# Performance work log

Hardware: AMD Instinct MI355X
Metric: run time of the kernel (lower is better)

Reference implementation:

```python
import jax, jax.numpy as jnp
import numpy as np

B_SZ = 4; SEQ = 2048; SPLIT = 1024
D_MODEL = 512; N_LAYERS = 2; EXPAND = 2
D_INNER = EXPAND * D_MODEL          # 1024
HEADDIM = 64; NHEADS = D_INNER // HEADDIM   # 16
DSTATE = 64; CONV = 4; CHUNK = 256
D_INPROJ = 2 * D_INNER + 2 * DSTATE + NHEADS   # z, xBC, dt
CONVDIM = D_INNER + 2 * DSTATE
NHID = 1024; NOUT = 10; CA_HEADS = 4; CA_HD = D_MODEL // CA_HEADS


def _ln(x, w, b, eps=1e-5):
    m = jnp.mean(x, -1, keepdims=True)
    v = jnp.mean(jnp.square(x - m), -1, keepdims=True)
    return (x - m) * jax.lax.rsqrt(v + eps) * w + b


def _segsum(x):
    # x: (..., T) -> (..., T, T) lower-triangular cumulative segment sums
    T = x.shape[-1]
    xc = jnp.cumsum(x, -1)
    ss = xc[..., :, None] - xc[..., None, :]
    mask = jnp.tril(jnp.ones((T, T), bool))
    return jnp.where(mask, ss, -jnp.inf)


def _ssd(x, A, B, C):
    # chunked SSD (Mamba2). x:(b,l,h,p) dt-prescaled; A:(b,l,h)=dt*A; B,C:(b,l,n)
    b, l, h, p = x.shape
    n = B.shape[-1]
    c = l // CHUNK
    x = x.reshape(b, c, CHUNK, h, p)
    A = jnp.transpose(A.reshape(b, c, CHUNK, h), (0, 1, 3, 2))   # (b,c,h,L)
    B = B.reshape(b, c, CHUNK, n)
    C = C.reshape(b, c, CHUNK, n)
    A_cum = jnp.cumsum(A, -1)
    Lmat = jnp.exp(_segsum(A))                                    # (b,c,h,L,L)
    Y_diag = jnp.einsum('bcln,bcsn,bchls,bcshp->bclhp', C, B, Lmat, x)
    decay_states = jnp.exp(A_cum[..., -1:] - A_cum)               # (b,c,h,L)
    states = jnp.einsum('bcln,bchl,bclhp->bchpn', B, decay_states, x)
    chunk_decay = jnp.exp(A_cum[..., -1])                         # (b,c,h)
    def step(hprev, inp):
        dec, s = inp
        return hprev * dec[..., None, None] + s, hprev
    init = jnp.zeros((b, h, p, n), x.dtype)
    _, prev = jax.lax.scan(step, init,
                           (jnp.moveaxis(chunk_decay, 1, 0), jnp.moveaxis(states, 1, 0)))
    prev = jnp.moveaxis(prev, 0, 1)                               # (b,c,h,p,n) state at chunk start
    Y_off = jnp.einsum('bcln,bchpn,bchl->bclhp', C, prev, jnp.exp(A_cum))
    return (Y_diag + Y_off).reshape(b, l, h, p)


def _mamba2_dir(u, Win, cw, cb, dtb, Alog, Dp, gw, Wout):
    b, l, _ = u.shape
    zxbcdt = u @ Win
    z, xBC, dt_raw = jnp.split(zxbcdt, [D_INNER, D_INNER + CONVDIM], -1)
    # causal depthwise conv, kernel CONV
    xp = jnp.pad(xBC, ((0, 0), (CONV - 1, 0), (0, 0)))
    xc = cb + sum(xp[:, k:k + l, :] * cw[:, k] for k in range(CONV))
    xc = jax.nn.silu(xc)
    x, Bm, Cm = jnp.split(xc, [D_INNER, D_INNER + DSTATE], -1)
    dt = jax.nn.softplus(dt_raw + dtb)                            # (b,l,h)
    A = -jnp.exp(Alog)                                            # (h,)
    xh = x.reshape(b, l, NHEADS, HEADDIM)
    y = _ssd(xh * dt[..., None], dt * A, Bm, Cm) + Dp[None, None, :, None] * xh
    y = y.reshape(b, l, D_INNER) * jax.nn.silu(z)                 # gated
    y = y * jax.lax.rsqrt(jnp.mean(jnp.square(y), -1, keepdims=True) + 1e-5) * gw
    return y @ Wout


def _cross_attn(q_in, c_in, nqw, nqb, nkvw, nkvb, qw, qb, kw, kb, vw, vb, ow, ob):
    res = q_in
    q = _ln(q_in, nqw, nqb)
    c = _ln(c_in, nkvw, nkvb)
    Bq, Nq, D = q.shape
    Nc = c.shape[1]
    Q = (q @ qw + qb).reshape(Bq, Nq, CA_HEADS, CA_HD)
    K = (c @ kw + kb).reshape(Bq, Nc, CA_HEADS, CA_HD)
    V = (c @ vw + vb).reshape(Bq, Nc, CA_HEADS, CA_HD)
    attn = jax.nn.softmax(jnp.einsum('bqhd,bkhd->bhqk', Q, K) / np.float32(np.sqrt(CA_HD)), -1)
    out = jnp.einsum('bhqk,bkhd->bqhd', attn, V).reshape(Bq, Nq, D)
    return res + out @ ow + ob


def _forward(x_enc, split_pos, in_proj_w, conv_w, conv_b, dt_bias, A_log, D_param,
             gnorm_w, out_proj_w, norm_w, norm_b, normf_w, normf_b,
             ca_nq_w, ca_nq_b, ca_nkv_w, ca_nkv_b, ca_qw, ca_qb, ca_kw, ca_kb,
             ca_vw, ca_vb, ca_ow, ca_ob, qp_w, qp_b, cp_w, cp_b,
             dec1_w, dec1_b, dec2_w, dec2_b):
    h = x_enc
    res = None
    for i in range(N_LAYERS):
        res = h if res is None else h + res
        hn = _ln(res, norm_w[i], norm_b[i])
        fwd = _mamba2_dir(hn, in_proj_w[i, 0], conv_w[i, 0], conv_b[i, 0], dt_bias[i, 0],
                          A_log[i, 0], D_param[i, 0], gnorm_w[i, 0], out_proj_w[i, 0])
        bwd = _mamba2_dir(jnp.flip(hn, 1), in_proj_w[i, 1], conv_w[i, 1], conv_b[i, 1],
                          dt_bias[i, 1], A_log[i, 1], D_param[i, 1], gnorm_w[i, 1], out_proj_w[i, 1])
        h = fwd + jnp.flip(bwd, 1)
    res = h + res
    h = _ln(res, normf_w, normf_b)
    context = h[:, :split_pos]
    query = h[:, split_pos:]
    q = query @ qp_w + qp_b
    c = context @ cp_w + cp_b
    out = _cross_attn(q, c, ca_nq_w, ca_nq_b, ca_nkv_w, ca_nkv_b,
                      ca_qw, ca_qb, ca_kw, ca_kb, ca_vw, ca_vb, ca_ow, ca_ob)
    out = jax.nn.gelu(out @ dec1_w + dec1_b, approximate=False) @ dec2_w + dec2_b
    return out


def setup_inputs() -> dict:
    key = jax.random.key(0)
    ks = iter(jax.random.split(key, 64))
    def nrm(shape, scale=0.02):
        return jax.random.normal(next(ks), shape, jnp.float32) * scale
    L2 = (N_LAYERS, 2)
    inp = {}
    inp['x_enc'] = jax.random.normal(next(ks), (B_SZ, SEQ, D_MODEL), jnp.float32)
    inp['split_pos'] = SPLIT
    inp['in_proj_w'] = nrm(L2 + (D_MODEL, D_INPROJ))
    inp['conv_w'] = nrm(L2 + (CONVDIM, CONV), 0.1)
    inp['conv_b'] = jnp.zeros(L2 + (CONVDIM,), jnp.float32)
    inp['dt_bias'] = nrm(L2 + (NHEADS,), 0.5)
    inp['A_log'] = jnp.log(jnp.broadcast_to(jnp.arange(1, NHEADS + 1, dtype=jnp.float32), L2 + (NHEADS,)))
    inp['D_param'] = jnp.ones(L2 + (NHEADS,), jnp.float32)
    inp['gnorm_w'] = jnp.ones(L2 + (D_INNER,), jnp.float32)
    inp['out_proj_w'] = nrm(L2 + (D_INNER, D_MODEL))
    inp['norm_w'] = jnp.ones((N_LAYERS, D_MODEL), jnp.float32)
    inp['norm_b'] = jnp.zeros((N_LAYERS, D_MODEL), jnp.float32)
    inp['normf_w'] = jnp.ones((D_MODEL,), jnp.float32)
    inp['normf_b'] = jnp.zeros((D_MODEL,), jnp.float32)
    inp['ca_nq_w'] = jnp.ones((D_MODEL,), jnp.float32); inp['ca_nq_b'] = jnp.zeros((D_MODEL,), jnp.float32)
    inp['ca_nkv_w'] = jnp.ones((D_MODEL,), jnp.float32); inp['ca_nkv_b'] = jnp.zeros((D_MODEL,), jnp.float32)
    for nm in ['ca_qw', 'ca_kw', 'ca_vw', 'ca_ow']:
        inp[nm] = nrm((D_MODEL, D_MODEL))
    for nm in ['ca_qb', 'ca_kb', 'ca_vb', 'ca_ob']:
        inp[nm] = jnp.zeros((D_MODEL,), jnp.float32)
    inp['qp_w'] = nrm((D_MODEL, D_MODEL)); inp['qp_b'] = jnp.zeros((D_MODEL,), jnp.float32)
    inp['cp_w'] = nrm((D_MODEL, D_MODEL)); inp['cp_b'] = jnp.zeros((D_MODEL,), jnp.float32)
    inp['dec1_w'] = nrm((D_MODEL, NHID)); inp['dec1_b'] = jnp.zeros((NHID,), jnp.float32)
    inp['dec2_w'] = nrm((NHID, NOUT)); inp['dec2_b'] = jnp.zeros((NOUT,), jnp.float32)
    return inp


def reference(x_enc, split_pos, in_proj_w, conv_w, conv_b, dt_bias, A_log, D_param,
              gnorm_w, out_proj_w, norm_w, norm_b, normf_w, normf_b,
              ca_nq_w, ca_nq_b, ca_nkv_w, ca_nkv_b, ca_qw, ca_qb, ca_kw, ca_kb,
              ca_vw, ca_vb, ca_ow, ca_ob, qp_w, qp_b, cp_w, cp_b,
              dec1_w, dec1_b, dec2_w, dec2_b):
    return _forward(x_enc, split_pos, in_proj_w, conv_w, conv_b, dt_bias, A_log, D_param,
                    gnorm_w, out_proj_w, norm_w, norm_b, normf_w, normf_b,
                    ca_nq_w, ca_nq_b, ca_nkv_w, ca_nkv_b, ca_qw, ca_qb, ca_kw, ca_kb,
                    ca_vw, ca_vb, ca_ow, ca_ob, qp_w, qp_b, cp_w, cp_b,
                    dec1_w, dec1_b, dec2_w, dec2_b)
```

## Files before the change

kernel.cpp:

```cpp
#include <hip/hip_runtime.h>
#include <hip/hip_bf16.h>

#define BS 4
#define SEQL 2048
#define DM 512
#define DIN 1024
#define NH 16
#define HD 64
#define DST 64
#define NC 8
#define CKS 256
#define DIP 2192
#define CVD 1152
#define NROWS (BS*SEQL)
#define NTOK (BS*SEQL*DM)

typedef unsigned short u16;
typedef __bf16 bf16x8 __attribute__((ext_vector_type(8)));
typedef float f32x4 __attribute__((ext_vector_type(4)));

__device__ __forceinline__ u16 cvt_bf16(float f){
  unsigned int x = __float_as_uint(f);
  unsigned int r = x + 0x7fffu + ((x>>16)&1u);
  return (u16)(r>>16);
}
__device__ __forceinline__ float bf2f(u16 u){
  return __uint_as_float(((unsigned int)u)<<16);
}

__global__ void k_add_flip(float* __restrict__ dst, const float* __restrict__ src, int flip){
  int i = blockIdx.x*256 + threadIdx.x;
  if(i >= NTOK) return;
  int d = i & (DM-1);
  int l = (i >> 9) & (SEQL-1);
  int b = i >> 20;
  int sl = flip ? (SEQL-1-l) : l;
  dst[i] += src[(b*SEQL + sl)*DM + d];
}

__global__ void k_flip(float* __restrict__ dst, const float* __restrict__ src){
  int i = blockIdx.x*256 + threadIdx.x;
  if(i >= NTOK) return;
  int d = i & (DM-1);
  int l = (i >> 9) & (SEQL-1);
  int b = i >> 20;
  dst[i] = src[(b*SEQL + (SEQL-1-l))*DM + d];
}

__global__ void k_cvt(const float* __restrict__ src, u16* __restrict__ dst, int n4){
  int i = blockIdx.x*256 + threadIdx.x;
  if(i >= n4) return;
  float4 f = reinterpret_cast<const float4*>(src)[i];
  ushort4 o; o.x=cvt_bf16(f.x); o.y=cvt_bf16(f.y); o.z=cvt_bf16(f.z); o.w=cvt_bf16(f.w);
  reinterpret_cast<ushort4*>(dst)[i] = o;
}

__global__ void k_ln(const float* __restrict__ X, const float* __restrict__ w,
                     const float* __restrict__ bb, float* __restrict__ O){
  int row = blockIdx.x, tid = threadIdx.x;
  const float* x = X + (size_t)row*DM;
  float* o = O + (size_t)row*DM;
  float s=0.f, s2=0.f;
  for(int j=tid;j<DM;j+=256){ float v=x[j]; s+=v; s2+=v*v; }
  __shared__ float r1[256], r2[256];
  r1[tid]=s; r2[tid]=s2; __syncthreads();
  for(int off=128;off>0;off>>=1){
    if(tid<off){ r1[tid]+=r1[tid+off]; r2[tid]+=r2[tid+off]; }
    __syncthreads();
  }
  float m = r1[0]*(1.f/DM);
  float var = r2[0]*(1.f/DM) - m*m;
  float inv = rsqrtf(var + 1e-5f);
  for(int j=tid;j<DM;j+=256) o[j] = (x[j]-m)*inv*w[j] + bb[j];
}

__global__ void k_rmsb(const float* __restrict__ Y, const float* __restrict__ gw,
                       u16* __restrict__ Obf){
  int row = blockIdx.x, tid = threadIdx.x;
  const float* y = Y + (size_t)row*DIN;
  float ss=0.f;
  for(int j=tid;j<DIN;j+=256){ float v=y[j]; ss+=v*v; }
  __shared__ float red[256];
  red[tid]=ss; __syncthreads();
  for(int off=128;off>0;off>>=1){
    if(tid<off) red[tid]+=red[tid+off];
    __syncthreads();
  }
  float inv = rsqrtf(red[0]*(1.f/DIN) + 1e-5f);
  for(int j=tid;j<DIN;j+=256) Obf[(size_t)row*DIN + j] = cvt_bf16(y[j]*inv*gw[j]);
}

__global__ void k_dec2(const float* __restrict__ D1, const float* __restrict__ w,
                       const float* __restrict__ bb, float* __restrict__ out){
  int row = blockIdx.x, tid = threadIdx.x;
  int lane = tid & 63, wave = tid >> 6;
  const float* x = D1 + (size_t)row*1024;
  float acc[10];
  #pragma unroll
  for(int o=0;o<10;o++) acc[o]=0.f;
  for(int j=tid;j<1024;j+=256){
    float v = x[j];
    const float* wr = w + (size_t)j*10;
    #pragma unroll
    for(int o=0;o<10;o++) acc[o] += v*wr[o];
  }
  __shared__ float red[4][10];
  #pragma unroll
  for(int o=0;o<10;o++){
    float v = acc[o];
    #pragma unroll
    for(int s=32;s>0;s>>=1) v += __shfl_down(v, s, 64);
    if(lane==0) red[wave][o] = v;
  }
  __syncthreads();
  if(tid < 10)
    out[(size_t)row*10 + tid] = red[0][tid]+red[1][tid]+red[2][tid]+red[3][tid] + bb[tid];
}

__global__ void k_wt2(const float* __restrict__ src, u16* __restrict__ dst,
                      int K, int N, int lds){
  __shared__ float t[32][33];
  int n0 = blockIdx.x*32, k0 = blockIdx.y*32;
  int tx = threadIdx.x, ty = threadIdx.y;
  #pragma unroll
  for(int i=0;i<32;i+=8){
    int k = k0+ty+i, n = n0+tx;
    t[ty+i][tx] = (n<N) ? src[(size_t)k*lds+n] : 0.f;
  }
  __syncthreads();
  #pragma unroll
  for(int i=0;i<32;i+=8){
    int n = n0+ty+i, k = k0+tx;
    if(n<N) dst[(size_t)n*K+k] = cvt_bf16(t[tx][ty+i]);
  }
}

__global__ void k_vtb(const float* __restrict__ VV, u16* __restrict__ VT){
  __shared__ float t[32][33];
  int z = blockIdx.z, b = z>>2, h = z&3;
  const float* src = VV + (size_t)b*524288 + h*128;
  u16* dst = VT + (size_t)z*131072;
  int n0 = blockIdx.x*32, k0 = blockIdx.y*32;
  int tx = threadIdx.x, ty = threadIdx.y;
  #pragma unroll
  for(int i=0;i<32;i+=8){
    int k = k0+ty+i, n = n0+tx;
    t[ty+i][tx] = src[(size_t)k*512+n];
  }
  __syncthreads();
  #pragma unroll
  for(int i=0;i<32;i+=8){
    int n = n0+ty+i, k = k0+tx;
    dst[(size_t)n*1024+k] = cvt_bf16(t[tx][ty+i]);
  }
}

__global__ void k_xdtt(const float* __restrict__ XC, const float* __restrict__ DT,
                       u16* __restrict__ XdT){
  __shared__ float t[32][33];
  int z = blockIdx.z;
  int h = z & 15, bc = z >> 4;
  int b = bc >> 3, c = bc & 7;
  int p0 = blockIdx.x*32, s0 = blockIdx.y*32;
  int tx = threadIdx.x, ty = threadIdx.y;
  int gbase = b*SEQL + c*CKS;
  #pragma unroll
  for(int i=0;i<32;i+=8){
    int s = s0+ty+i, p = p0+tx;
    int g = gbase + s;
    t[ty+i][tx] = XC[(size_t)g*CVD + h*HD + p] * DT[(size_t)g*NH + h];
  }
  __syncthreads();
  u16* dst = XdT + (size_t)z*16384;
  #pragma unroll
  for(int i=0;i<32;i+=8){
    int p = p0+ty+i, s = s0+tx;
    dst[(size_t)p*256 + s] = cvt_bf16(t[tx][ty+i]);
  }
}

__global__ void k_btc(const u16* __restrict__ Bbf, u16* __restrict__ BTc){
  __shared__ u16 t[32][33];
  int bc = blockIdx.z;
  const u16* src = Bbf + (size_t)bc*16384;
  u16* dst = BTc + (size_t)bc*16384;
  int n0 = blockIdx.x*32, l0 = blockIdx.y*32;
  int tx = threadIdx.x, ty = threadIdx.y;
  #pragma unroll
  for(int i=0;i<32;i+=8){
    int l = l0+ty+i, n = n0+tx;
    t[ty+i][tx] = src[(size_t)l*64+n];
  }
  __syncthreads();
  #pragma unroll
  for(int i=0;i<32;i+=8){
    int n = n0+ty+i, l = l0+tx;
    dst[(size_t)n*256+l] = t[tx][ty+i];
  }
}

__global__ __launch_bounds__(256) void k_mg(
    const u16* __restrict__ A, const u16* __restrict__ BT,
    float* __restrict__ C, int M, int N, int K, int lda, int ldb, int ldc)
{
  __shared__ u16 As[128*32];
  __shared__ u16 Bs[128*32];
  const int tid = threadIdx.x;
  const int row0 = blockIdx.y*128, col0 = blockIdx.x*128;
  const int lane = tid & 63, wave = tid >> 6;
  const int wm = wave >> 1, wn = wave & 1;
  const int lr = lane & 15, ksg = (lane >> 4);
  const int srow = lane >> 2;
  const int slot = lane & 3;
  f32x4 acc[4][4];
  #pragma unroll
  for(int i=0;i<4;i++)
    #pragma unroll
    for(int j=0;j<4;j++) acc[i][j] = (f32x4){0.f,0.f,0.f,0.f};
  for(int k0=0;k0<K;k0+=32){
    #pragma unroll
    for(int i=0;i<2;i++){
      int seg = wave*2 + i;
      int row = seg*16 + srow;
      int kk  = slot ^ ((row>>1)&3);
      const u16* ga = A + (size_t)(row0+row)*lda + k0 + kk*8;
      __builtin_amdgcn_global_load_lds(
        (const __attribute__((address_space(1))) void*)ga,
        (__attribute__((address_space(3))) void*)&As[seg*512], 16, 0, 0);
      int bcol = col0 + row; if(bcol > N-1) bcol = N-1;
      const u16* gb = BT + (size_t)bcol*ldb + k0 + kk*8;
      __builtin_amdgcn_global_load_lds(
        (const __attribute__((address_space(1))) void*)gb,
        (__attribute__((address_space(3))) void*)&Bs[seg*512], 16, 0, 0);
    }
    __syncthreads();
    bf16x8 afr[4], bfr[4];
    #pragma unroll
    for(int i=0;i<4;i++){
      int ar = wm*64+i*16+lr;
      afr[i] = *reinterpret_cast<const bf16x8*>(&As[ar*32 + (ksg^((ar>>1)&3))*8]);
    }
    #pragma unroll
    for(int j=0;j<4;j++){
      int br = wn*64+j*16+lr;
      bfr[j] = *reinterpret_cast<const bf16x8*>(&Bs[br*32 + (ksg^((br>>1)&3))*8]);
    }
    #pragma unroll
    for(int i=0;i<4;i++)
      #pragma unroll
      for(int j=0;j<4;j++)
        acc[i][j] = __builtin_amdgcn_mfma_f32_16x16x32_bf16(afr[i], bfr[j], acc[i][j], 0, 0, 0);
    __syncthreads();
  }
  const int hi = lane >> 4, lo = lane & 15;
  #pragma unroll
  for(int i=0;i<4;i++)
    #pragma unroll
    for(int j=0;j<4;j++)
      #pragma unroll
      for(int r=0;r<4;r++){
        int row = row0 + wm*64 + i*16 + 4*hi + r;
        int col = col0 + wn*64 + j*16 + lo;
        if(col < N) C[(size_t)row*ldc + col] = acc[i][j][r];
      }
}

__global__ __launch_bounds__(256) void k_mgo(
    const u16* __restrict__ A, const u16* __restrict__ BT,
    float* __restrict__ H, int flip)
{
  const int N = 512, K = 1024;
  __shared__ u16 As[128*32];
  __shared__ u16 Bs[128*32];
  const int tid = threadIdx.x;
  const int row0 = blockIdx.y*128, col0 = blockIdx.x*128;
  const int lane = tid & 63, wave = tid >> 6;
  const int wm = wave >> 1, wn = wave & 1;
  const int lr = lane & 15, ksg = (lane >> 4);
  const int srow = lane >> 2;
  const int slot = lane & 3;
  f32x4 acc[4][4];
  #pragma unroll
  for(int i=0;i<4;i++)
    #pragma unroll
    for(int j=0;j<4;j++) acc[i][j] = (f32x4){0.f,0.f,0.f,0.f};
  for(int k0=0;k0<K;k0+=32){
    #pragma unroll
    for(int i=0;i<2;i++){
      int seg = wave*2 + i;
      int row = seg*16 + srow;
      int kk  = slot ^ ((row>>1)&3);
      const u16* ga = A + (size_t)(row0+row)*K + k0 + kk*8;
      __builtin_amdgcn_global_load_lds(
        (const __attribute__((address_space(1))) void*)ga,
        (__attribute__((address_space(3))) void*)&As[seg*512], 16, 0, 0);
      int bcol = col0 + row; if(bcol > N-1) bcol = N-1;
      const u16* gb = BT + (size_t)bcol*K + k0 + kk*8;
      __builtin_amdgcn_global_load_lds(
        (const __attribute__((address_space(1))) void*)gb,
        (__attribute__((address_space(3))) void*)&Bs[seg*512], 16, 0, 0);
    }
    __syncthreads();
    bf16x8 afr[4], bfr[4];
    #pragma unroll
    for(int i=0;i<4;i++){
      int ar = wm*64+i*16+lr;
      afr[i] = *reinterpret_cast<const bf16x8*>(&As[ar*32 + (ksg^((ar>>1)&3))*8]);
    }
    #pragma unroll
    for(int j=0;j<4;j++){
      int br = wn*64+j*16+lr;
      bfr[j] = *reinterpret_cast<const bf16x8*>(&Bs[br*32 + (ksg^((br>>1)&3))*8]);
    }
    #pragma unroll
    for(int i=0;i<4;i++)
      #pragma unroll
      for(int j=0;j<4;j++)
        acc[i][j] = __builtin_amdgcn_mfma_f32_16x16x32_bf16(afr[i], bfr[j], acc[i][j], 0, 0, 0);
    __syncthreads();
  }
  const int hi = lane >> 4, lo = lane & 15;
  #pragma unroll
  for(int i=0;i<4;i++)
    #pragma unroll
    for(int j=0;j<4;j++)
      #pragma unroll
      for(int r=0;r<4;r++){
        int row = row0 + wm*64 + i*16 + 4*hi + r;
        int col = col0 + wn*64 + j*16 + lo;
        if(col < N){
          int b = row >> 11, l = row & (SEQL-1);
          int sl = flip ? (SEQL-1-l) : l;
          size_t ci = (size_t)(b*SEQL + sl)*DM + col;
          H[ci] += acc[i][j][r];
        }
      }
}

__global__ __launch_bounds__(256) void k_mgb(
    const u16* __restrict__ A0, const u16* __restrict__ BT0,
    float* __restrict__ C0, int M, int N, int K, int lda, int ldb, int ldc,
    long sAz, long sBz, long sCo, long sCi, int shC)
{
  const int z = blockIdx.z;
  const u16* A  = A0  + (size_t)z*sAz;
  const u16* BT = BT0 + (size_t)z*sBz;
  float* C = C0 + (size_t)(z>>shC)*sCo + (size_t)(z & ((1<<shC)-1))*sCi;
  __shared__ uint4 As4[128*5];
  __shared__ uint4 Bs4[128*5];
  const int tid = threadIdx.x;
  const int row0 = blockIdx.y*128, col0 = blockIdx.x*128;
  const int lane = tid & 63, wave = tid >> 6;
  const int wm = wave >> 1, wn = wave & 1;
  const int lr = lane & 15, ksg = (lane >> 4);
  f32x4 acc[4][4];
  #pragma unroll
  for(int i=0;i<4;i++)
    #pragma unroll
    for(int j=0;j<4;j++) acc[i][j] = (f32x4){0.f,0.f,0.f,0.f};
  for(int k0=0;k0<K;k0+=32){
    #pragma unroll
    for(int i=0;i<2;i++){
      int t2 = tid + i*256;
      int rr = t2 >> 2, sg = (t2 & 3);
      uint4 av = *reinterpret_cast<const uint4*>(A + (size_t)(row0+rr)*lda + k0 + sg*8);
      uint4 bv = {0u,0u,0u,0u};
      if(col0+rr < N) bv = *reinterpret_cast<const uint4*>(BT + (size_t)(col0+rr)*ldb + k0 + sg*8);
      As4[rr*5 + sg] = av;
      Bs4[rr*5 + sg] = bv;
    }
    __syncthreads();
    bf16x8 afr[4], bfr[4];
    #pragma unroll
    for(int i=0;i<4;i++) afr[i] = *reinterpret_cast<const bf16x8*>(&As4[(wm*64+i*16+lr)*5 + ksg]);
    #pragma unroll
    for(int j=0;j<4;j++) bfr[j] = *reinterpret_cast<const bf16x8*>(&Bs4[(wn*64+j*16+lr)*5 + ksg]);
    #pragma unroll
    for(int i=0;i<4;i++)
      #pragma unroll
      for(int j=0;j<4;j++)
        acc[i][j] = __builtin_amdgcn_mfma_f32_16x16x32_bf16(afr[i], bfr[j], acc[i][j], 0, 0, 0);
    __syncthreads();
  }
  const int hi = lane >> 4, lo = lane & 15;
  #pragma unroll
  for(int i=0;i<4;i++)
    #pragma unroll
    for(int j=0;j<4;j++)
      #pragma unroll
      for(int r=0;r<4;r++){
        int row = row0 + wm*64 + i*16 + 4*hi + r;
        int col = col0 + wn*64 + j*16 + lo;
        if(col < N) C[(size_t)row*ldc + col] = acc[i][j][r];
      }
}

__global__ __launch_bounds__(256) void k_mgg(
    const float* __restrict__ Sf, const float* __restrict__ ACUM,
    const u16* __restrict__ XdT, float* __restrict__ Y)
{
  const int z = blockIdx.z;
  const int h = z & 15, bc = z >> 4;
  const int b = bc >> 3, c = bc & 7;
  const float* Az = Sf + (size_t)bc*65536;
  const float* Acp = ACUM + (size_t)z*256;
  const u16* BT = XdT + (size_t)z*16384;
  float* Cp = Y + (size_t)b*2097152 + (size_t)c*262144 + h*64;
  __shared__ uint4 As4[128*5];
  __shared__ uint4 Bs4[128*5];
  __shared__ float AcS[256];
  const int tid = threadIdx.x;
  AcS[tid] = Acp[tid];
  __syncthreads();
  const int row0 = blockIdx.y*128;
  const int lane = tid & 63, wave = tid >> 6;
  const int wm = wave >> 1, wn = wave & 1;
  const int lr = lane & 15, ksg = (lane >> 4);
  f32x4 acc[4][4];
  #pragma unroll
  for(int i=0;i<4;i++)
    #pragma unroll
    for(int j=0;j<4;j++) acc[i][j] = (f32x4){0.f,0.f,0.f,0.f};
  for(int k0=0;k0<256;k0+=32){
    #pragma unroll
    for(int i=0;i<2;i++){
      int t2 = tid + i*256;
      int rr = t2 >> 2, sg = (t2 & 3);
      int l = row0 + rr;
      int sbase = k0 + sg*8;
      float4 v0 = *reinterpret_cast<const float4*>(Az + (size_t)l*256 + sbase);
      float4 v1 = *reinterpret_cast<const float4*>(Az + (size_t)l*256 + sbase + 4);
      float acl = AcS[l];
      float vv[8] = {v0.x,v0.y,v0.z,v0.w,v1.x,v1.y,v1.z,v1.w};
      u16 gbuf[8];
      #pragma unroll
      for(int e=0;e<8;e++){
        int s = sbase + e;
        float g = 0.f;
        if(s <= l) g = __expf(acl - AcS[s]) * vv[e];
        gbuf[e] = cvt_bf16(g);
      }
      As4[rr*5 + sg] = *reinterpret_cast<uint4*>(gbuf);
      uint4 bv = {0u,0u,0u,0u};
      if(rr < 64) bv = *reinterpret_cast<const uint4*>(BT + (size_t)rr*256 + sbase);
      Bs4[rr*5 + sg] = bv;
    }
    __syncthreads();
    bf16x8 afr[4], bfr[4];
    #pragma unroll
    for(int i=0;i<4;i++) afr[i] = *reinterpret_cast<const bf16x8*>(&As4[(wm*64+i*16+lr)*5 + ksg]);
    #pragma unroll
    for(int j=0;j<4;j++) bfr[j] = *reinterpret_cast<const bf16x8*>(&Bs4[(wn*64+j*16+lr)*5 + ksg]);
    #pragma unroll
    for(int i=0;i<4;i++)
      #pragma unroll
      for(int j=0;j<4;j++)
        acc[i][j] = __builtin_amdgcn_mfma_f32_16x16x32_bf16(afr[i], bfr[j], acc[i][j], 0, 0, 0);
    __syncthreads();
  }
  const int hi = lane >> 4, lo = lane & 15;
  #pragma unroll
  for(int i=0;i<4;i++)
    #pragma unroll
    for(int j=0;j<4;j++)
      #pragma unroll
      for(int r=0;r<4;r++){
        int row = row0 + wm*64 + i*16 + 4*hi + r;
        int col = wn*64 + j*16 + lo;
        if(col < 64) Cp[(size_t)row*1024 + col] = acc[i][j][r];
      }
}

__global__ __launch_bounds__(256) void k_mgs(
    const u16* __restrict__ XdT, const u16* __restrict__ BTc,
    const float* __restrict__ ACUM, float* __restrict__ ST)
{
  const int z = blockIdx.z;
  const int bc = z >> 4;
  const u16* Ap = XdT + (size_t)z*16384;
  const u16* BT = BTc + (size_t)bc*16384;
  float* Cp = ST + (size_t)z*4096;
  __shared__ uint4 As4[128*5];
  __shared__ uint4 Bs4[128*5];
  __shared__ float decS[256];
  const int tid = threadIdx.x;
  {
    const float* Acp = ACUM + (size_t)z*256;
    decS[tid] = __expf(Acp[255] - Acp[tid]);
  }
  __syncthreads();
  const int lane = tid & 63, wave = tid >> 6;
  const int wm = wave >> 1, wn = wave & 1;
  const int lr = lane & 15, ksg = (lane >> 4);
  f32x4 acc[4][4];
  #pragma unroll
  for(int i=0;i<4;i++)
    #pragma unroll
    for(int j=0;j<4;j++) acc[i][j] = (f32x4){0.f,0.f,0.f,0.f};
  for(int k0=0;k0<256;k0+=32){
    #pragma unroll
    for(int i=0;i<2;i++){
      int t2 = tid + i*256;
      int rr = t2 >> 2, sg = (t2 & 3);
      int sbase = k0 + sg*8;
      uint4 av = {0u,0u,0u,0u};
      if(rr < 64){
        uint4 raw = *reinterpret_cast<const uint4*>(Ap + (size_t)rr*256 + sbase);
        const u16* rp = reinterpret_cast<const u16*>(&raw);
        u16 buf[8];
        #pragma unroll
        for(int e=0;e<8;e++) buf[e] = cvt_bf16(bf2f(rp[e]) * decS[sbase+e]);
        av = *reinterpret_cast<uint4*>(buf);
      }
      As4[rr*5 + sg] = av;
      uint4 bv = {0u,0u,0u,0u};
      if(rr < 64) bv = *reinterpret_cast<const uint4*>(BT + (size_t)rr*256 + sbase);
      Bs4[rr*5 + sg] = bv;
    }
    __syncthreads();
    bf16x8 afr[4], bfr[4];
    #pragma unroll
    for(int i=0;i<4;i++) afr[i] = *reinterpret_cast<const bf16x8*>(&As4[(wm*64+i*16+lr)*5 + ksg]);
    #pragma unroll
    for(int j=0;j<4;j++) bfr[j] = *reinterpret_cast<const bf16x8*>(&Bs4[(wn*64+j*16+lr)*5 + ksg]);
    #pragma unroll
    for(int i=0;i<4;i++)
      #pragma unroll
      for(int j=0;j<4;j++)
        acc[i][j] = __builtin_amdgcn_mfma_f32_16x16x32_bf16(afr[i], bfr[j], acc[i][j], 0, 0, 0);
    __syncthreads();
  }
  const int hi = lane >> 4, lo = lane & 15;
  #pragma unroll
  for(int i=0;i<4;i++)
    #pragma unroll
    for(int j=0;j<4;j++)
      #pragma unroll
      for(int r=0;r<4;r++){
        int row = wm*64 + i*16 + 4*hi + r;
        int col = wn*64 + j*16 + lo;
        if(row < 64 && col < 64) Cp[(size_t)row*64 + col] = acc[i][j][r];
      }
}

__global__ __launch_bounds__(256) void k_mgab(
    const u16* __restrict__ A0, const u16* __restrict__ BT0,
    float* __restrict__ C0, u16* __restrict__ Cb0,
    int M, int N, int K, int lda, int ldb, int ldc,
    long sAo, long sAi, long sBo, long sBi, long sCo, long sCi, float scale)
{
  const int z = blockIdx.z;
  const u16* A  = A0  + (size_t)(z>>2)*sAo + (size_t)(z&3)*sAi;
  const u16* BT = BT0 + (size_t)(z>>2)*sBo + (size_t)(z&3)*sBi;
  const size_t offC = (size_t)(z>>2)*sCo + (size_t)(z&3)*sCi;
  __shared__ uint4 As4[128*5];
  __shared__ uint4 Bs4[128*5];
  const int tid = threadIdx.x;
  const int row0 = blockIdx.y*128, col0 = blockIdx.x*128;
  const int lane = tid & 63, wave = tid >> 6;
  const int wm = wave >> 1, wn = wave & 1;
  const int lr = lane & 15, ksg = (lane >> 4);
  f32x4 acc[4][4];
  #pragma unroll
  for(int i=0;i<4;i++)
    #pragma unroll
    for(int j=0;j<4;j++) acc[i][j] = (f32x4){0.f,0.f,0.f,0.f};
  for(int k0=0;k0<K;k0+=32){
    #pragma unroll
    for(int i=0;i<2;i++){
      int t2 = tid + i*256;
      int rr = t2 >> 2, sg = (t2 & 3);
      uint4 av = *reinterpret_cast<const uint4*>(A + (size_t)(row0+rr)*lda + k0 + sg*8);
      uint4 bv = {0u,0u,0u,0u};
      if(col0+rr < N) bv = *reinterpret_cast<const uint4*>(BT + (size_t)(col0+rr)*ldb + k0 + sg*8);
      As4[rr*5 + sg] = av;
      Bs4[rr*5 + sg] = bv;
    }
    __syncthreads();
    bf16x8 afr[4], bfr[4];
    #pragma unroll
    for(int i=0;i<4;i++) afr[i] = *reinterpret_cast<const bf16x8*>(&As4[(wm*64+i*16+lr)*5 + ksg]);
    #pragma unroll
    for(int j=0;j<4;j++) bfr[j] = *reinterpret_cast<const bf16x8*>(&Bs4[(wn*64+j*16+lr)*5 + ksg]);
    #pragma unroll
    for(int i=0;i<4;i++)
      #pragma unroll
      for(int j=0;j<4;j++)
        acc[i][j] = __builtin_amdgcn_mfma_f32_16x16x32_bf16(afr[i], bfr[j], acc[i][j], 0, 0, 0);
    __syncthreads();
  }
  const int hi = lane >> 4, lo = lane & 15;
  #pragma unroll
  for(int i=0;i<4;i++)
    #pragma unroll
    for(int j=0;j<4;j++)
      #pragma unroll
      for(int r=0;r<4;r++){
        int row = row0 + wm*64 + i*16 + 4*hi + r;
        int col = col0 + wn*64 + j*16 + lo;
        if(col < N){
          float v = acc[i][j][r] * scale;
          size_t ci = offC + (size_t)row*ldc + col;
          if(C0) C0[ci] = v;
          else   Cb0[ci] = cvt_bf16(v);
        }
      }
}

__global__ __launch_bounds__(256) void k_mgy(
    const u16* __restrict__ Cb0, const u16* __restrict__ PV0,
    const float* __restrict__ ACUM, const float* __restrict__ XCp,
    const float* __restrict__ ZBp, const float* __restrict__ Dp,
    float* __restrict__ Y)
{
  const int z = blockIdx.z;
  const int b = z>>3, c = z&7;
  const u16* A  = Cb0 + (size_t)z*16384;
  const u16* BT = PV0 + (size_t)z*65536;
  const int N = 1024;
  __shared__ uint4 As4[128*5];
  __shared__ uint4 Bs4[128*5];
  const int tid = threadIdx.x;
  const int row0 = blockIdx.y*128, col0 = blockIdx.x*128;
  const int lane = tid & 63, wave = tid >> 6;
  const int wm = wave >> 1, wn = wave & 1;
  const int lr = lane & 15, ksg = (lane >> 4);
  f32x4 acc[4][4];
  #pragma unroll
  for(int i=0;i<4;i++)
    #pragma unroll
    for(int j=0;j<4;j++) acc[i][j] = (f32x4){0.f,0.f,0.f,0.f};
  for(int k0=0;k0<64;k0+=32){
    #pragma unroll
    for(int i=0;i<2;i++){
      int t2 = tid + i*256;
      int rr = t2 >> 2, sg = (t2 & 3);
      uint4 av = *reinterpret_cast<const uint4*>(A + (size_t)(row0+rr)*64 + k0 + sg*8);
      uint4 bv = {0u,0u,0u,0u};
      if(col0+rr < N) bv = *reinterpret_cast<const uint4*>(BT + (size_t)(col0+rr)*64 + k0 + sg*8);
      As4[rr*5 + sg] = av;
      Bs4[rr*5 + sg] = bv;
    }
    __syncthreads();
    bf16x8 afr[4], bfr[4];
    #pragma unroll
    for(int i=0;i<4;i++) afr[i] = *reinterpret_cast<const bf16x8*>(&As4[(wm*64+i*16+lr)*5 + ksg]);
    #pragma unroll
    for(int j=0;j<4;j++) bfr[j] = *reinterpret_cast<const bf16x8*>(&Bs4[(wn*64+j*16+lr)*5 + ksg]);
    #pragma unroll
    for(int i=0;i<4;i++)
      #pragma unroll
      for(int j=0;j<4;j++)
        acc[i][j] = __builtin_amdgcn_mfma_f32_16x16x32_bf16(afr[i], bfr[j], acc[i][j], 0, 0, 0);
    __syncthreads();
  }
  const int hi = lane >> 4, lo = lane & 15;
  #pragma unroll
  for(int i=0;i<4;i++)
    #pragma unroll
    for(int j=0;j<4;j++)
      #pragma unroll
      for(int r=0;r<4;r++){
        int row = row0 + wm*64 + i*16 + 4*hi + r;
        int col = col0 + wn*64 + j*16 + lo;
        int h = col >> 6;
        int g = b*SEQL + c*CKS + row;
        float ac = ACUM[((size_t)z*NH + h)*CKS + row];
        float xh = XCp[(size_t)g*CVD + col];
        float zg = ZBp[(size_t)g*DIP + col];
        size_t ci = (size_t)g*DIN + col;
        float v = Y[ci] + expf(ac)*acc[i][j][r] + Dp[h]*xh;
        float sig = 1.f/(1.f+expf(-zg));
        Y[ci] = v * (zg*sig);
      }
}

__global__ __launch_bounds__(256) void k_mge(
    const u16* __restrict__ A, const u16* __restrict__ BT,
    const float* __restrict__ bias, const float* __restrict__ res,
    float* __restrict__ C, u16* __restrict__ Cbf,
    int M, int N, int K, int lda, int ldb, int ldc, float scale, int act)
{
  __shared__ uint4 As4[128*5];
  __shared__ uint4 Bs4[128*5];
  const int tid = threadIdx.x;
  const int row0 = blockIdx.y*128, col0 = blockIdx.x*128;
  const int lane = tid & 63, wave = tid >> 6;
  const int wm = wave >> 1, wn = wave & 1;
  const int lr = lane & 15, ksg = (lane >> 4);
  f32x4 acc[4][4];
  #pragma unroll
  for(int i=0;i<4;i++)
    #pragma unroll
    for(int j=0;j<4;j++) acc[i][j] = (f32x4){0.f,0.f,0.f,0.f};
  for(int k0=0;k0<K;k0+=32){
    #pragma unroll
    for(int i=0;i<2;i++){
      int t2 = tid + i*256;
      int rr = t2 >> 2, sg = (t2 & 3);
      uint4 av = *reinterpret_cast<const uint4*>(A + (size_t)(row0+rr)*lda + k0 + sg*8);
      uint4 bv = {0u,0u,0u,0u};
      if(col0+rr < N) bv = *reinterpret_cast<const uint4*>(BT + (size_t)(col0+rr)*ldb + k0 + sg*8);
      As4[rr*5 + sg] = av;
      Bs4[rr*5 + sg] = bv;
    }
    __syncthreads();
    bf16x8 afr[4], bfr[4];
    #pragma unroll
    for(int i=0;i<4;i++) afr[i] = *reinterpret_cast<const bf16x8*>(&As4[(wm*64+i*16+lr)*5 + ksg]);
    #pragma unroll
    for(int j=0;j<4;j++) bfr[j] = *reinterpret_cast<const bf16x8*>(&Bs4[(wn*64+j*16+lr)*5 + ksg]);
    #pragma unroll
    for(int i=0;i<4;i++)
      #pragma unroll
      for(int j=0;j<4;j++)
        acc[i][j] = __builtin_amdgcn_mfma_f32_16x16x32_bf16(afr[i], bfr[j], acc[i][j], 0, 0, 0);
    __syncthreads();
  }
  const int hi = lane >> 4, lo = lane & 15;
  #pragma unroll
  for(int i=0;i<4;i++)
    #pragma unroll
    for(int j=0;j<4;j++)
      #pragma unroll
      for(int r=0;r<4;r++){
        int row = row0 + wm*64 + i*16 + 4*hi + r;
        int col = col0 + wn*64 + j*16 + lo;
        if(col < N){
          float v = acc[i][j][r];
          if(bias) v += bias[col];
          v *= scale;
          if(act==1) v = 0.5f*v*(1.f+erff(v*0.70710678118654752f));
          size_t ci = (size_t)row*ldc + col;
          if(res) v += res[ci];
          if(C) C[ci] = v;
          else  Cbf[ci] = cvt_bf16(v);
        }
      }
}

__global__ void k_sm(u16* __restrict__ S){
  size_t row = blockIdx.x;
  u16* p = S + row*1024;
  int tid = threadIdx.x;
  ushort4 u = reinterpret_cast<ushort4*>(p)[tid];
  float v0=bf2f(u.x), v1=bf2f(u.y), v2=bf2f(u.z), v3=bf2f(u.w);
  float m = fmaxf(fmaxf(v0,v1),fmaxf(v2,v3));
  __shared__ float red[256];
  red[tid]=m; __syncthreads();
  for(int o=128;o>0;o>>=1){ if(tid<o) red[tid]=fmaxf(red[tid],red[tid+o]); __syncthreads(); }
  m = red[0]; __syncthreads();
  v0=__expf(v0-m); v1=__expf(v1-m); v2=__expf(v2-m); v3=__expf(v3-m);
  float s = v0+v1+v2+v3;
  red[tid]=s; __syncthreads();
  for(int o=128;o>0;o>>=1){ if(tid<o) red[tid]+=red[tid+o]; __syncthreads(); }
  float inv = 1.f/red[0];
  ushort4 o4; o4.x=cvt_bf16(v0*inv); o4.y=cvt_bf16(v1*inv); o4.z=cvt_bf16(v2*inv); o4.w=cvt_bf16(v3*inv);
  reinterpret_cast<ushort4*>(p)[tid] = o4;
}

__global__ void k_conv4(const float* __restrict__ ZB, const float* __restrict__ cw,
                        const float* __restrict__ cb, float* __restrict__ XC){
  int i = blockIdx.x*256 + threadIdx.x;
  if(i >= BS*512*CVD) return;
  int cch = i % CVD;
  int lq = (i / CVD) & 511;
  int b = i / (CVD*512);
  int l0 = lq*4;
  float w[7];
  #pragma unroll
  for(int t=0;t<7;t++){
    int sl = l0 - 3 + t;
    w[t] = (sl >= 0) ? ZB[(size_t)(b*SEQL+sl)*DIP + DIN + cch] : 0.f;
  }
  float c0 = cw[cch*4+0], c1 = cw[cch*4+1], c2 = cw[cch*4+2], c3 = cw[cch*4+3];
  float bb2 = cb[cch];
  #pragma unroll
  for(int j=0;j<4;j++){
    float v = bb2 + w[j]*c0 + w[j+1]*c1 + w[j+2]*c2 + w[j+3]*c3;
    float sig = 1.f/(1.f+expf(-v));
    XC[(size_t)(b*SEQL + l0 + j)*CVD + cch] = v*sig;
  }
}

__global__ void k_dt(const float* __restrict__ ZB, const float* __restrict__ dtb,
                     const float* __restrict__ Alog, float* __restrict__ DT,
                     float* __restrict__ DA){
  int i = blockIdx.x*256 + threadIdx.x;
  if(i >= BS*SEQL*NH) return;
  int h = i & (NH-1);
  int row = i >> 4;
  float raw = ZB[(size_t)row*DIP + (DIN+CVD) + h] + dtb[h];
  float dt = fmaxf(raw,0.f) + log1pf(expf(-fabsf(raw)));
  DT[i] = dt;
  DA[i] = dt * (-expf(Alog[h]));
}

__global__ void k_acum(const float* __restrict__ DA, float* __restrict__ ACUM,
                       float* __restrict__ CDEC){
  int blk = blockIdx.x;
  int h = blk & 15, c = (blk>>4)&7, b = blk>>7;
  int l = threadIdx.x;
  __shared__ float s[256];
  int gl = c*CKS + l;
  s[l] = DA[(size_t)(b*SEQL + gl)*NH + h];
  __syncthreads();
  for(int off=1; off<256; off<<=1){
    float v = (l>=off) ? s[l-off] : 0.f;
    __syncthreads();
    s[l] += v;
    __syncthreads();
  }
  ACUM[(size_t)blk*CKS + l] = s[l];
  if(l==255) CDEC[blk] = expf(s[255]);
}

__global__ void k_bc(const float* __restrict__ XC, u16* __restrict__ Bbf,
                     u16* __restrict__ Cbf){
  int i = blockIdx.x*256 + threadIdx.x;
  if(i >= NROWS*DST) return;
  int g = i >> 6, n = i & 63;
  Bbf[i] = cvt_bf16(XC[(size_t)g*CVD + DIN + n]);
  Cbf[i] = cvt_bf16(XC[(size_t)g*CVD + DIN + DST + n]);
}

__global__ void k_scan(const float* __restrict__ ST, const float* __restrict__ CDEC,
                       float* __restrict__ PREV){
  int i = blockIdx.x*256 + threadIdx.x;
  if(i >= BS*NH*4096) return;
  int pn = i & 4095;
  int h = (i>>12) & 15;
  int b = i >> 16;
  float run = 0.f;
  for(int c=0;c<8;c++){
    size_t idx = (size_t)((b*8+c)*16+h)*4096 + pn;
    PREV[idx] = run;
    run = run*CDEC[(b*8+c)*16+h] + ST[idx];
  }
}

__global__ void k_extract(const float* __restrict__ HF, float* __restrict__ QIN,
                          float* __restrict__ CIN){
  int i = blockIdx.x*256 + threadIdx.x;
  if(i >= BS*1024*DM) return;
  int d = i & (DM-1);
  int q = (i>>9) & 1023;
  int b = i >> 19;
  QIN[i] = HF[(size_t)(b*SEQL + 1024 + q)*DM + d];
  CIN[i] = HF[(size_t)(b*SEQL + q)*DM + d];
}

extern "C" void kernel_launch(void* const* d_in, const int* in_sizes, int n_in,
                              void* d_out, int out_size, void* d_ws, size_t ws_size,
                              hipStream_t stream) {
  (void)in_sizes; (void)n_in; (void)out_size; (void)ws_size;
  const float* x_enc     = (const float*)d_in[0];
  const float* in_proj_w = (const float*)d_in[2];
  const float* conv_w    = (const float*)d_in[3];
  const float* conv_b    = (const float*)d_in[4];
  const float* dt_bias   = (const float*)d_in[5];
  const float* A_log     = (const float*)d_in[6];
  const float* D_param   = (const float*)d_in[7];
  const float* gnorm_w   = (const float*)d_in[8];
  const float* out_proj_w= (const float*)d_in[9];
  const float* norm_w    = (const float*)d_in[10];
  const float* norm_b    = (const float*)d_in[11];
  const float* normf_w   = (const float*)d_in[12];
  const float* normf_b   = (const float*)d_in[13];
  const float* ca_nq_w   = (const float*)d_in[14];
  const float* ca_nq_b   = (const float*)d_in[15];
  const float* ca_nkv_w  = (const float*)d_in[16];
  const float* ca_nkv_b  = (const float*)d_in[17];
  const float* ca_qw     = (const float*)d_in[18];
  const float* ca_kw     = (const float*)d_in[19];
  const float* ca_vw     = (const float*)d_in[20];
  const float* ca_ow     = (const float*)d_in[21];
  const float* ca_qb     = (const float*)d_in[22];
  const float* ca_kb     = (const float*)d_in[23];
  const float* ca_vb     = (const float*)d_in[24];
  const float* ca_ob     = (const float*)d_in[25];
  const float* qp_w      = (const float*)d_in[26];
  const float* qp_b      = (const float*)d_in[27];
  const float* cp_w      = (const float*)d_in[28];
  const float* cp_b      = (const float*)d_in[29];
  const float* dec1_w    = (const float*)d_in[30];
  const float* dec1_b    = (const float*)d_in[31];
  const float* dec2_w    = (const float*)d_in[32];
  const float* dec2_b    = (const float*)d_in[33];

  float* W = (float*)d_ws;
  size_t off = 0;
  auto alloc = [&](size_t n){ float* pp = W + off; off += n; return pp; };
  float* RES  = alloc((size_t)NTOK);
  float* H    = alloc((size_t)NTOK);
  float* HN   = alloc((size_t)NTOK);
  float* HNF  = alloc((size_t)NTOK);
  float* ZB   = alloc((size_t)NROWS*DIP);
  float* XC   = alloc((size_t)NROWS*CVD);
  float* DT   = alloc((size_t)NROWS*NH);
  float* DA   = alloc((size_t)NROWS*NH);
  float* ACUM = alloc((size_t)BS*NC*NH*CKS);
  float* CDEC = alloc((size_t)BS*NC*NH);
  float* Y    = alloc((size_t)NROWS*DIN);
  float* ST   = alloc((size_t)BS*NC*NH*4096);
  float* PREV = alloc((size_t)BS*NC*NH*4096);
  float* YD   = alloc((size_t)NTOK);
  float* HF   = alloc((size_t)NTOK);

  u16* Ubf    = (u16*)HF;
  u16* WinTc  = (u16*)(HF + 2097152);
  u16* WoutTc = (u16*)(HF + 2097152 + 561152);
  u16* Ybf    = (u16*)HNF;
  u16*   Bbf    = (u16*)HNF;
  u16*   Cbf    = Bbf + 524288;
  float* Sf     = HNF + 524288;
  u16*   PREVbf = (u16*)Sf;
  u16*   BTc    = (u16*)(HNF + 2621440);
  u16*   XdTg   = (u16*)YD;

  const int TPB = 256;
  const int gTok = (NTOK+TPB-1)/TPB;
  dim3 tb(32,8);

  hipMemcpyAsync(RES, x_enc, (size_t)NTOK*4, hipMemcpyDeviceToDevice, stream);

  for(int layer=0; layer<2; ++layer){
    if(layer>0) k_add_flip<<<gTok,TPB,0,stream>>>(RES, H, 0);
    k_ln<<<NROWS,TPB,0,stream>>>(RES, norm_w + layer*DM, norm_b + layer*DM, HN);
    hipMemsetAsync(H, 0, (size_t)NTOK*4, stream);
    for(int dir=0; dir<2; ++dir){
      int idx = layer*2 + dir;
      const float* cw   = conv_w   + (size_t)idx*CVD*4;
      const float* cb   = conv_b   + (size_t)idx*CVD;
      const float* dtb  = dt_bias  + (size_t)idx*NH;
      const float* Alog = A_log    + (size_t)idx*NH;
      const float* Dp   = D_param  + (size_t)idx*NH;
      const float* gw   = gnorm_w  + (size_t)idx*DIN;

      if(dir==0){
        k_cvt<<<(NTOK/4+TPB-1)/TPB,TPB,0,stream>>>(HN, Ubf, NTOK/4);
      }else{
        k_flip<<<gTok,TPB,0,stream>>>(HNF, HN);
        k_cvt<<<(NTOK/4+TPB-1)/TPB,TPB,0,stream>>>(HNF, Ubf, NTOK/4);
      }
      k_wt2<<<dim3(69,16),tb,0,stream>>>(in_proj_w + (size_t)idx*DM*DIP, WinTc, 512, 2192, 2192);
      k_mg<<<dim3(18,64),256,0,stream>>>(Ubf, WinTc, ZB, 8192, 2192, 512, 512, 512, 2192);

      k_conv4<<<(BS*512*CVD+TPB-1)/TPB,TPB,0,stream>>>(ZB, cw, cb, XC);
      k_dt<<<(BS*SEQL*NH+TPB-1)/TPB,TPB,0,stream>>>(ZB, dtb, Alog, DT, DA);
      k_acum<<<BS*NC*NH,256,0,stream>>>(DA, ACUM, CDEC);

      k_bc<<<(NROWS*DST+TPB-1)/TPB,TPB,0,stream>>>(XC, Bbf, Cbf);
      k_mgb<<<dim3(2,2,32),256,0,stream>>>(Cbf, Bbf, Sf,
            256, 256, 64, 64, 64, 256, 16384, 16384, 65536, 0, 0);
      k_xdtt<<<dim3(2,8,512),tb,0,stream>>>(XC, DT, XdTg);
      k_mgg<<<dim3(1,2,512),256,0,stream>>>(Sf, ACUM, XdTg, Y);

      k_btc<<<dim3(2,8,32),tb,0,stream>>>(Bbf, BTc);
      k_mgs<<<dim3(1,1,512),256,0,stream>>>(XdTg, BTc, ACUM, ST);
      k_scan<<<(BS*NH*4096+TPB-1)/TPB,TPB,0,stream>>>(ST, CDEC, PREV);
      k_cvt<<<(2097152/4+TPB-1)/TPB,TPB,0,stream>>>(PREV, PREVbf, 2097152/4);
      k_mgy<<<dim3(8,2,32),256,0,stream>>>(Cbf, PREVbf, ACUM, XC, ZB, Dp, Y);

      k_rmsb<<<NROWS,256,0,stream>>>(Y, gw, Ybf);
      k_wt2<<<dim3(16,32),tb,0,stream>>>(out_proj_w + (size_t)idx*DIN*DM, WoutTc, 1024, 512, 512);
      k_mgo<<<dim3(4,64),256,0,stream>>>(Ybf, WoutTc, H, dir);
    }
  }
  k_add_flip<<<gTok,TPB,0,stream>>>(RES, H, 0);
  k_ln<<<NROWS,TPB,0,stream>>>(RES, normf_w, normf_b, HF);

  float* P0   = ZB;
  float* QIN  = P0 + 0;
  float* CIN  = P0 + 2097152;
  float* QPb  = P0 + 4194304;
  float* CPb  = P0 + 6291456;
  float* QN   = P0 + 8388608;
  float* CN   = P0 + 10485760;
  float* AO   = P0 + 12582912;
  float* O1   = P0 + 14680064;
  float* D1   = P0 + 16777216;
  float* VV   = D1;
  u16* U0     = (u16*)(P0 + 20971520);
  u16* Qbf    = U0 + 0;
  u16* Cbf2   = U0 + 2097152;
  u16* QNbf   = U0 + 4194304;
  u16* CNbf   = U0 + 6291456;
  u16* QQbf   = U0 + 8388608;
  u16* KKbf   = U0 + 10485760;
  u16* VTbf   = U0 + 12582912;
  u16* AObf   = U0 + 14680064;
  u16* O1bf   = U0 + 16777216;
  u16* qpT    = U0 + 18874368;
  u16* cpT    = qpT + 262144;
  u16* qwT    = qpT + 524288;
  u16* kwT    = qpT + 786432;
  u16* vwT    = qpT + 1048576;
  u16* owT    = qpT + 1310720;
  u16* dec1T  = qpT + 1572864;
  u16* Pbf    = qpT + 2097152;

  const int M2 = BS*1024;
  k_extract<<<(BS*1024*DM+TPB-1)/TPB,TPB,0,stream>>>(HF, QIN, CIN);
  k_cvt<<<(2097152/4+TPB-1)/TPB,TPB,0,stream>>>(QIN, Qbf, 2097152/4);
  k_cvt<<<(2097152/4+TPB-1)/TPB,TPB,0,stream>>>(CIN, Cbf2, 2097152/4);
  k_wt2<<<dim3(16,16),tb,0,stream>>>(qp_w, qpT, 512, 512, 512);
  k_wt2<<<dim3(16,16),tb,0,stream>>>(cp_w, cpT, 512, 512, 512);
  k_wt2<<<dim3(16,16),tb,0,stream>>>(ca_qw, qwT, 512, 512, 512);
  k_wt2<<<dim3(16,16),tb,0,stream>>>(ca_kw, kwT, 512, 512, 512);
  k_wt2<<<dim3(16,16),tb,0,stream>>>(ca_vw, vwT, 512, 512, 512);
  k_wt2<<<dim3(16,16),tb,0,stream>>>(ca_ow, owT, 512, 512, 512);
  k_wt2<<<dim3(32,16),tb,0,stream>>>(dec1_w, dec1T, 512, 1024, 1024);

  k_mge<<<dim3(4,32),256,0,stream>>>(Qbf, qpT, qp_b, nullptr, QPb, nullptr,
                                     M2, 512, 512, 512, 512, 512, 1.f, 0);
  k_mge<<<dim3(4,32),256,0,stream>>>(Cbf2, cpT, cp_b, nullptr, CPb, nullptr,
                                     M2, 512, 512, 512, 512, 512, 1.f, 0);
  k_ln<<<M2,TPB,0,stream>>>(QPb, ca_nq_w, ca_nq_b, QN);
  k_ln<<<M2,TPB,0,stream>>>(CPb, ca_nkv_w, ca_nkv_b, CN);
  k_cvt<<<(2097152/4+TPB-1)/TPB,TPB,0,stream>>>(QN, QNbf, 2097152/4);
  k_cvt<<<(2097152/4+TPB-1)/TPB,TPB,0,stream>>>(CN, CNbf, 2097152/4);
  k_mge<<<dim3(4,32),256,0,stream>>>(QNbf, qwT, ca_qb, nullptr, nullptr, QQbf,
                                     M2, 512, 512, 512, 512, 512, 1.f, 0);
  k_mge<<<dim3(4,32),256,0,stream>>>(CNbf, kwT, ca_kb, nullptr, nullptr, KKbf,
                                     M2, 512, 512, 512, 512, 512, 1.f, 0);
  k_mge<<<dim3(4,32),256,0,stream>>>(CNbf, vwT, ca_vb, nullptr, VV, nullptr,
                                     M2, 512, 512, 512, 512, 512, 1.f, 0);
  k_vtb<<<dim3(4,32,16),tb,0,stream>>>(VV, VTbf);
  const float scl = 0.088388347648318447f;
  k_mgab<<<dim3(8,8,16),256,0,stream>>>(QQbf, KKbf, nullptr, Pbf,
        1024, 1024, 128, 512, 512, 1024,
        524288, 128, 524288, 128, 4194304, 1048576, scl);
  k_sm<<<16384,256,0,stream>>>(Pbf);
  k_mgab<<<dim3(1,8,16),256,0,stream>>>(Pbf, VTbf, AO, nullptr,
        1024, 128, 1024, 1024, 1024, 512,
        4194304, 1048576, 524288, 131072, 524288, 128, 1.f);
  k_cvt<<<(2097152/4+TPB-1)/TPB,TPB,0,stream>>>(AO, AObf, 2097152/4);
  k_mge<<<dim3(4,32),256,0,stream>>>(AObf, owT, ca_ob, QPb, O1, nullptr,
                                     M2, 512, 512, 512, 512, 512, 1.f, 0);
  k_cvt<<<(2097152/4+TPB-1)/TPB,TPB,0,stream>>>(O1, O1bf, 2097152/4);
  k_mge<<<dim3(8,32),256,0,stream>>>(O1bf, dec1T, dec1_b, nullptr, D1, nullptr,
                                     M2, 1024, 512, 512, 512, 1024, 1.f, 1);
  k_dec2<<<M2,256,0,stream>>>(D1, dec2_w, dec2_b, (float*)d_out);
}
```

Measured before the change: 1.338 ms.

## Fuse intra-chunk SSD GEMM with inter-chunk state GEMM and gating epilogue

Merges the diagonal-block kernel (k_mgg) and the off-diagonal state-output kernel (k_mgy) into one kernel. It accumulates both GEMMs into the same registers, folding the exp(A_cum) row scale into the C operand, and applies the D-skip and SiLU gating in the epilogue. This removes one launch and a full fp32 Y write-then-read round trip. PREVbf moves to its own buffer so it no longer aliases Sf, which the fused kernel still reads. In exchange, the second GEMM now runs per head with K=64 and small N, and rescaling C to bf16 adds some rounding.

```diff
diff --git a/kernel.cpp b/kernel.cpp
--- a/kernel.cpp
+++ b/kernel.cpp
@@ -395,17 +395,21 @@
       }
 }
 
-__global__ __launch_bounds__(256) void k_mgg(
+__global__ __launch_bounds__(256) void k_mgf(
     const float* __restrict__ Sf, const float* __restrict__ ACUM,
-    const u16* __restrict__ XdT, float* __restrict__ Y)
+    const u16* __restrict__ XdT, const u16* __restrict__ Cb0,
+    const u16* __restrict__ PV0, const float* __restrict__ XCp,
+    const float* __restrict__ ZBp, const float* __restrict__ Dp,
+    float* __restrict__ Y)
 {
   const int z = blockIdx.z;
   const int h = z & 15, bc = z >> 4;
   const int b = bc >> 3, c = bc & 7;
   const float* Az = Sf + (size_t)bc*65536;
   const float* Acp = ACUM + (size_t)z*256;
-  const u16* BT = XdT + (size_t)z*16384;
-  float* Cp = Y + (size_t)b*2097152 + (size_t)c*262144 + h*64;
+  const u16* BT1 = XdT + (size_t)z*16384;
+  const u16* A2  = Cb0 + (size_t)bc*16384;
+  const u16* BT2 = PV0 + (size_t)bc*65536 + (size_t)h*4096;
   __shared__ uint4 As4[128*5];
   __shared__ uint4 Bs4[128*5];
   __shared__ float AcS[256];
@@ -442,7 +446,37 @@
       }
       As4[rr*5 + sg] = *reinterpret_cast<uint4*>(gbuf);
       uint4 bv = {0u,0u,0u,0u};
-      if(rr < 64) bv = *reinterpret_cast<const uint4*>(BT + (size_t)rr*256 + sbase);
+      if(rr < 64) bv = *reinterpret_cast<const uint4*>(BT1 + (size_t)rr*256 + sbase);
+      Bs4[rr*5 + sg] = bv;
+    }
+    __syncthreads();
+    bf16x8 afr[4], bfr[4];
+    #pragma unroll
+    for(int i=0;i<4;i++) afr[i] = *reinterpret_cast<const bf16x8*>(&As4[(wm*64+i*16+lr)*5 + ksg]);
+    #pragma unroll
+    for(int j=0;j<4;j++) bfr[j] = *reinterpret_cast<const bf16x8*>(&Bs4[(wn*64+j*16+lr)*5 + ksg]);
+    #pragma unroll
+    for(int i=0;i<4;i++)
+      #pragma unroll
+      for(int j=0;j<4;j++)
+        acc[i][j] = __builtin_amdgcn_mfma_f32_16x16x32_bf16(afr[i], bfr[j], acc[i][j], 0, 0, 0);
+    __syncthreads();
+  }
+  for(int k0=0;k0<64;k0+=32){
+    #pragma unroll
+    for(int i=0;i<2;i++){
+      int t2 = tid + i*256;
+      int rr = t2 >> 2, sg = (t2 & 3);
+      int sbase = k0 + sg*8;
+      uint4 raw = *reinterpret_cast<const uint4*>(A2 + (size_t)(row0+rr)*64 + sbase);
+      const u16* rp = reinterpret_cast<const u16*>(&raw);
+      float scale = __expf(AcS[row0+rr]);
+      u16 buf[8];
+      #pragma unroll
+      for(int e=0;e<8;e++) buf[e] = cvt_bf16(bf2f(rp[e]) * scale);
+      As4[rr*5 + sg] = *reinterpret_cast<uint4*>(buf);
+      uint4 bv = {0u,0u,0u,0u};
+      if(rr < 64) bv = *reinterpret_cast<const uint4*>(BT2 + (size_t)rr*64 + sbase);
       Bs4[rr*5 + sg] = bv;
     }
     __syncthreads();
@@ -467,7 +501,15 @@
       for(int r=0;r<4;r++){
         int row = row0 + wm*64 + i*16 + 4*hi + r;
         int col = wn*64 + j*16 + lo;
-        if(col < 64) Cp[(size_t)row*1024 + col] = acc[i][j][r];
+        if(col < 64){
+          int g = b*SEQL + c*CKS + row;
+          int ch = h*HD + col;
+          float xh = XCp[(size_t)g*CVD + ch];
+          float zg = ZBp[(size_t)g*DIP + ch];
+          float v = acc[i][j][r] + Dp[h]*xh;
+          float sig = 1.f/(1.f+expf(-zg));
+          Y[(size_t)g*DIN + ch] = v * (zg*sig);
+        }
       }
 }
 
@@ -604,74 +646,6 @@
           if(C0) C0[ci] = v;
           else   Cb0[ci] = cvt_bf16(v);
         }
-      }
-}
-
-__global__ __launch_bounds__(256) void k_mgy(
-    const u16* __restrict__ Cb0, const u16* __restrict__ PV0,
-    const float* __restrict__ ACUM, const float* __restrict__ XCp,
-    const float* __restrict__ ZBp, const float* __restrict__ Dp,
-    float* __restrict__ Y)
-{
-  const int z = blockIdx.z;
-  const int b = z>>3, c = z&7;
-  const u16* A  = Cb0 + (size_t)z*16384;
-  const u16* BT = PV0 + (size_t)z*65536;
-  const int N = 1024;
-  __shared__ uint4 As4[128*5];
-  __shared__ uint4 Bs4[128*5];
-  const int tid = threadIdx.x;
-  const int row0 = blockIdx.y*128, col0 = blockIdx.x*128;
-  const int lane = tid & 63, wave = tid >> 6;
-  const int wm = wave >> 1, wn = wave & 1;
-  const int lr = lane & 15, ksg = (lane >> 4);
-  f32x4 acc[4][4];
-  #pragma unroll
-  for(int i=0;i<4;i++)
-    #pragma unroll
-    for(int j=0;j<4;j++) acc[i][j] = (f32x4){0.f,0.f,0.f,0.f};
-  for(int k0=0;k0<64;k0+=32){
-    #pragma unroll
-    for(int i=0;i<2;i++){
-      int t2 = tid + i*256;
-      int rr = t2 >> 2, sg = (t2 & 3);
-      uint4 av = *reinterpret_cast<const uint4*>(A + (size_t)(row0+rr)*64 + k0 + sg*8);
-      uint4 bv = {0u,0u,0u,0u};
-      if(col0+rr < N) bv = *reinterpret_cast<const uint4*>(BT + (size_t)(col0+rr)*64 + k0 + sg*8);
-      As4[rr*5 + sg] = av;
-      Bs4[rr*5 + sg] = bv;
-    }
-    __syncthreads();
-    bf16x8 afr[4], bfr[4];
-    #pragma unroll
-    for(int i=0;i<4;i++) afr[i] = *reinterpret_cast<const bf16x8*>(&As4[(wm*64+i*16+lr)*5 + ksg]);
-    #pragma unroll
-    for(int j=0;j<4;j++) bfr[j] = *reinterpret_cast<const bf16x8*>(&Bs4[(wn*64+j*16+lr)*5 + ksg]);
-    #pragma unroll
-    for(int i=0;i<4;i++)
-      #pragma unroll
-      for(int j=0;j<4;j++)
-        acc[i][j] = __builtin_amdgcn_mfma_f32_16x16x32_bf16(afr[i], bfr[j], acc[i][j], 0, 0, 0);
-    __syncthreads();
-  }
-  const int hi = lane >> 4, lo = lane & 15;
-  #pragma unroll
-  for(int i=0;i<4;i++)
-    #pragma unroll
-    for(int j=0;j<4;j++)
-      #pragma unroll
-      for(int r=0;r<4;r++){
-        int row = row0 + wm*64 + i*16 + 4*hi + r;
-        int col = col0 + wn*64 + j*16 + lo;
-        int h = col >> 6;
-        int g = b*SEQL + c*CKS + row;
-        float ac = ACUM[((size_t)z*NH + h)*CKS + row];
-        float xh = XCp[(size_t)g*CVD + col];
-        float zg = ZBp[(size_t)g*DIP + col];
-        size_t ci = (size_t)g*DIN + col;
-        float v = Y[ci] + expf(ac)*acc[i][j][r] + Dp[h]*xh;
-        float sig = 1.f/(1.f+expf(-zg));
-        Y[ci] = v * (zg*sig);
       }
 }
 
@@ -914,8 +888,8 @@
   u16*   Bbf    = (u16*)HNF;
   u16*   Cbf    = Bbf + 524288;
   float* Sf     = HNF + 524288;
-  u16*   PREVbf = (u16*)Sf;
   u16*   BTc    = (u16*)(HNF + 2621440);
+  u16*   PREVbf = (u16*)(HNF + 2883584);
   u16*   XdTg   = (u16*)YD;
 
   const int TPB = 256;
@@ -954,13 +928,11 @@
       k_mgb<<<dim3(2,2,32),256,0,stream>>>(Cbf, Bbf, Sf,
             256, 256, 64, 64, 64, 256, 16384, 16384, 65536, 0, 0);
       k_xdtt<<<dim3(2,8,512),tb,0,stream>>>(XC, DT, XdTg);
-      k_mgg<<<dim3(1,2,512),256,0,stream>>>(Sf, ACUM, XdTg, Y);
-
       k_btc<<<dim3(2,8,32),tb,0,stream>>>(Bbf, BTc);
       k_mgs<<<dim3(1,1,512),256,0,stream>>>(XdTg, BTc, ACUM, ST);
       k_scan<<<(BS*NH*4096+TPB-1)/TPB,TPB,0,stream>>>(ST, CDEC, PREV);
       k_cvt<<<(2097152/4+TPB-1)/TPB,TPB,0,stream>>>(PREV, PREVbf, 2097152/4);
-      k_mgy<<<dim3(8,2,32),256,0,stream>>>(Cbf, PREVbf, ACUM, XC, ZB, Dp, Y);
+      k_mgf<<<dim3(1,2,512),256,0,stream>>>(Sf, ACUM, XdTg, Cbf, PREVbf, XC, ZB, Dp, Y);
 
       k_rmsb<<<NROWS,256,0,stream>>>(Y, gw, Ybf);
       k_wt2<<<dim3(16,32),tb,0,stream>>>(out_proj_w + (size_t)idx*DIN*DM, WoutTc, 1024, 512, 512);
```

Result: faster. 1.309 ms (-2.1%).
